# Kernel optimization log

Measured on AMD Instinct MI355X. Metric: run time of the kernel, lower is better.

Reference implementation:

```python
import jax, jax.numpy as jnp
import numpy as np

_CLIP = 1e4

def _n2n(t):
    return jnp.nan_to_num(t, nan=0.0, posinf=_CLIP, neginf=-_CLIP)

def setup_inputs() -> dict:
    key = jax.random.key(0)
    ks = jax.random.split(key, 9)
    B, N, E, DH, DM = 4, 16384, 65536, 128, 64
    s = 0.05
    return {
        "x": jax.random.normal(ks[0], (B, N, 3), jnp.float32),
        "h": jax.random.normal(ks[1], (B, N, DH), jnp.float32),
        "edge_index": jax.random.randint(ks[2], (B, E, 2), 0, N, jnp.int64 if jax.config.jax_enable_x64 else jnp.int32),
        "pe_w1": jax.random.normal(ks[3], (2 * DH + 1, DM), jnp.float32) * s,
        "pe_b1": jnp.zeros((DM,), jnp.float32),
        "pe_w2": jax.random.normal(ks[4], (DM, DM), jnp.float32) * s,
        "pe_b2": jnp.zeros((DM,), jnp.float32),
        "px_w": jax.random.normal(ks[5], (DM, 1), jnp.float32) * s,
        "ph_w1": jax.random.normal(ks[6], (DH + DM, DH), jnp.float32) * s,
        "ph_b1": jnp.zeros((DH,), jnp.float32),
        "ph_w2": jax.random.normal(ks[7], (DH, DH), jnp.float32) * s,
        "ph_b2": jnp.zeros((DH,), jnp.float32),
    }

def reference(x, h, edge_index, pe_w1, pe_b1, pe_w2, pe_b2, px_w, ph_w1, ph_b1, ph_w2, ph_b2):
    B = x.shape[0]
    src = edge_index[:, :, 0]          # [B,E]
    dst = edge_index[:, :, 1]
    bidx = jnp.arange(B)[:, None]      # [B,1] for batched gather/scatter
    x_i = x[bidx, src]                 # [B,E,3]
    x_j = x[bidx, dst]
    h_i = h[bidx, src]                 # [B,E,DH]
    h_j = h[bidx, dst]
    diff = x_i - x_j
    dist2 = jnp.clip((diff ** 2).sum(-1, keepdims=True), 1e-12, None)  # [B,E,1]
    edge_input = _n2n(jnp.concatenate([h_i, h_j, dist2], axis=-1))
    # phi_e: Linear -> SiLU -> Linear -> SiLU
    m = jax.nn.silu(edge_input @ pe_w1 + pe_b1)
    m_ij = _n2n(jax.nn.silu(m @ pe_w2 + pe_b2))   # [B,E,DM]
    m_x = m_ij @ px_w                             # [B,E,1]
    direction = diff / (jnp.sqrt(dist2) + 1e-8)
    delta_x_ij = _n2n(m_x * direction)            # [B,E,3]
    delta_x = jnp.zeros_like(x).at[bidx, src].add(delta_x_ij)
    delta_h_msg = jnp.zeros((B, x.shape[1], m_ij.shape[-1]), h.dtype).at[bidx, src].add(m_ij)
    h_input = jnp.concatenate([h, delta_h_msg], axis=-1)
    h_new = h + jax.nn.silu(h_input @ ph_w1 + ph_b1) @ ph_w2 + ph_b2
    x_new = x + delta_x
    return _n2n(x_new), _n2n(h_new)
```

## Files before the change

### kernel.cpp

```cpp
#include <hip/hip_runtime.h>


typedef unsigned short ushort_t;
typedef __attribute__((ext_vector_type(8))) short bf16x8;
typedef __attribute__((ext_vector_type(4))) float f32x4;
typedef _Float16 h2 __attribute__((ext_vector_type(2)));

__device__ __forceinline__ float fast_rcp(float v) { return __builtin_amdgcn_rcpf(v); }
__device__ __forceinline__ float fast_silu(float v) { return v * fast_rcp(1.0f + __expf(-v)); }
__device__ __forceinline__ ushort_t f2bf(float f) {
    unsigned u = __float_as_uint(f);
    u += 0x7fffu + ((u >> 16) & 1u);
    return (ushort_t)(u >> 16);
}
__device__ __forceinline__ float bf2f(ushort_t b) {
    return __uint_as_float(((unsigned)b) << 16);
}
__device__ __forceinline__ h2 u2h2(unsigned u) {
    union { unsigned u; h2 h; } v; v.u = u; return v.h;
}

__global__ __launch_bounds__(256) void init_k(const float* __restrict__ pe_w1,
                                              const float* __restrict__ pe_w2,
                                              const float* __restrict__ ph_w1,
                                              const float* __restrict__ ph_w2,
                                              int* __restrict__ cursor,
                                              ushort_t* __restrict__ W1t,
                                              ushort_t* __restrict__ Wp1t,
                                              ushort_t* __restrict__ Wp2t,
                                              unsigned* __restrict__ w2h) {
    int gg = blockIdx.x * 256 + threadIdx.x;
    if (gg < 65536) { cursor[gg] = 0; return; }
    int g = gg - 65536;
    if (g < 16384) {
        int c = g >> 7, k = g & 127;
        float v = (c < 64) ? pe_w1[k * 64 + c] : pe_w1[(128 + k) * 64 + (c - 64)];
        W1t[g] = f2bf(v);
    } else if (g < 40960) {
        int g2 = g - 16384;
        int n = g2 / 192, k = g2 - n * 192;
        Wp1t[g2] = f2bf(ph_w1[k * 128 + n]);
    } else if (g < 57344) {
        int g3 = g - 40960;
        int n = g3 >> 7, k = g3 & 127;
        Wp2t[g3] = f2bf(ph_w2[k * 128 + n]);
    } else if (g < 59392) {
        int g4 = g - 57344;
        int k2 = g4 >> 6, c = g4 & 63;
        union { unsigned u; _Float16 h[2]; } p;
        p.h[0] = (_Float16)pe_w2[(2 * k2) * 64 + c];
        p.h[1] = (_Float16)pe_w2[(2 * k2 + 1) * 64 + c];
        w2h[g4] = p.u;
    }
}

__global__ __launch_bounds__(256) void scatter_k(const int* __restrict__ ei,
                                                 int* __restrict__ cursor,
                                                 int* __restrict__ elist) {
    int e = blockIdx.x * 256 + threadIdx.x;
    int2 sd = ((const int2*)ei)[e];
    int b = e >> 16;
    int gi = (b << 14) + sd.x;
    int gj = (b << 14) + sd.y;
    int slot = atomicAdd(&cursor[gi], 1);
    if (slot < 64) elist[gi * 64 + slot] = gj;
}

__global__ __launch_bounds__(64, 4) void node_k(const float* __restrict__ x,
                                                const ushort_t* __restrict__ P,
                                                const int* __restrict__ cursor,
                                                const int* __restrict__ elist,
                                                const float* __restrict__ w1,
                                                const float* __restrict__ b1,
                                                const unsigned* __restrict__ w2h,
                                                const float* __restrict__ b2,
                                                const float* __restrict__ pxw,
                                                ushort_t* __restrict__ dh,
                                                float* __restrict__ outx) {
    const int n = blockIdx.x;
    const int lane = threadIdx.x;
    __shared__ __attribute__((aligned(16))) unsigned m_u[32];
    ushort_t* mh = (ushort_t*)m_u;

    const float w1r = w1[256 * 64 + lane];
    const float b2v = b2[lane];
    const float pxv = pxw[lane];
    const float Pib = bf2f(P[(size_t)n * 128 + lane]) + b1[lane];
    const float xi0 = x[n * 3 + 0];
    const float xi1 = x[n * 3 + 1];
    const float xi2 = x[n * 3 + 2];

    float dhacc = 0.0f;
    float dxp0 = 0.0f, dxp1 = 0.0f, dxp2 = 0.0f;
    const int dg = min(cursor[n], 64);
    const int base = n * 64;

    int gj0 = (dg > 0) ? elist[base] : 0;
    float Pj = bf2f(P[(size_t)gj0 * 128 + 64 + lane]);
    float xj0 = x[gj0 * 3 + 0];
    float xj1 = x[gj0 * 3 + 1];
    float xj2 = x[gj0 * 3 + 2];

    for (int t = 0; t < dg; t++) {
        int gjn = (t + 1 < dg) ? elist[base + t + 1] : 0;
        float Pjn = bf2f(P[(size_t)gjn * 128 + 64 + lane]);
        float xn0 = x[gjn * 3 + 0];
        float xn1 = x[gjn * 3 + 1];
        float xn2 = x[gjn * 3 + 2];

        float ddx = xi0 - xj0;
        float ddy = xi1 - xj1;
        float ddz = xi2 - xj2;
        float d2 = fmaxf(ddx * ddx + ddy * ddy + ddz * ddz, 1e-12f);
        float m = fast_silu(Pib + Pj + d2 * w1r);
        __builtin_amdgcn_wave_barrier();
        union { ushort_t s; _Float16 h; } mc;
        mc.h = (_Float16)m;
        mh[lane] = mc.s;
        __builtin_amdgcn_wave_barrier();
        float s0 = b2v, s1 = 0.0f, s2 = 0.0f, s3 = 0.0f;
#pragma unroll
        for (int q = 0; q < 8; q++) {
            uint4 mm = *(const uint4*)&m_u[q * 4];
            s0 = __builtin_amdgcn_fdot2(u2h2(mm.x), u2h2(w2h[(4 * q + 0) * 64 + lane]), s0, false);
            s1 = __builtin_amdgcn_fdot2(u2h2(mm.y), u2h2(w2h[(4 * q + 1) * 64 + lane]), s1, false);
            s2 = __builtin_amdgcn_fdot2(u2h2(mm.z), u2h2(w2h[(4 * q + 2) * 64 + lane]), s2, false);
            s3 = __builtin_amdgcn_fdot2(u2h2(mm.w), u2h2(w2h[(4 * q + 3) * 64 + lane]), s3, false);
        }
        __builtin_amdgcn_wave_barrier();
        float m2 = fast_silu((s0 + s1) + (s2 + s3));
        dhacc += m2;
        float c = m2 * pxv * fast_rcp(sqrtf(d2) + 1e-8f);
        dxp0 = fmaf(c, ddx, dxp0);
        dxp1 = fmaf(c, ddy, dxp1);
        dxp2 = fmaf(c, ddz, dxp2);

        Pj = Pjn; xj0 = xn0; xj1 = xn1; xj2 = xn2;
    }

    dh[(size_t)n * 64 + lane] = f2bf(dhacc);

    for (int off = 32; off; off >>= 1) {
        dxp0 += __shfl_down(dxp0, off);
        dxp1 += __shfl_down(dxp1, off);
        dxp2 += __shfl_down(dxp2, off);
    }
    if (lane == 0) {
        outx[n * 3 + 0] = xi0 + dxp0;
        outx[n * 3 + 1] = xi1 + dxp1;
        outx[n * 3 + 2] = xi2 + dxp2;
    }
}

template <bool EMIT_BF16>
__global__ __launch_bounds__(256, 2) void pgemm_k(const float* __restrict__ A0,
                                                  const ushort_t* __restrict__ Wt,
                                                  ushort_t* __restrict__ outP,
                                                  ushort_t* __restrict__ hbout) {
    constexpr int KPAD = 40;
    __shared__ ushort_t As[128 * KPAD];
    __shared__ ushort_t Bs[128 * KPAD];
    const int tid = threadIdx.x;
    const int m0 = blockIdx.x * 128;
    const int wave = tid >> 6;
    const int lane = tid & 63;
    const int lr = lane & 15;
    const int lq = lane >> 4;

    f32x4 acc[2][8];
#pragma unroll
    for (int mt = 0; mt < 2; mt++)
#pragma unroll
        for (int nt = 0; nt < 8; nt++) { f32x4 z = {0.f,0.f,0.f,0.f}; acc[mt][nt] = z; }

    for (int k0 = 0; k0 < 128; k0 += 32) {
#pragma unroll
        for (int i = 0; i < 4; i++) {
            int lin = tid + i * 256;
            int m = lin >> 3;
            int kq = (lin & 7) * 4;
            float4 v = *(const float4*)(A0 + (size_t)(m0 + m) * 128 + k0 + kq);
            ushort4 w4;
            w4.x = f2bf(v.x); w4.y = f2bf(v.y); w4.z = f2bf(v.z); w4.w = f2bf(v.w);
            if (EMIT_BF16)
                *(ushort4*)(hbout + (size_t)(m0 + m) * 128 + k0 + kq) = w4;
            *(ushort4*)&As[m * KPAD + kq] = w4;
        }
#pragma unroll
        for (int i = 0; i < 2; i++) {
            int lin = tid + i * 256;
            int n = lin >> 2;
            int kq = (lin & 3) * 8;
            *(uint4*)&Bs[n * KPAD + kq] = *(const uint4*)(Wt + (size_t)n * 128 + k0 + kq);
        }
        __syncthreads();
        bf16x8 af[2], bfr[8];
#pragma unroll
        for (int mt = 0; mt < 2; mt++)
            af[mt] = *(const bf16x8*)&As[(wave * 32 + mt * 16 + lr) * KPAD + lq * 8];
#pragma unroll
        for (int nt = 0; nt < 8; nt++)
            bfr[nt] = *(const bf16x8*)&Bs[(nt * 16 + lr) * KPAD + lq * 8];
#pragma unroll
        for (int mt = 0; mt < 2; mt++)
#pragma unroll
            for (int nt = 0; nt < 8; nt++)
                acc[mt][nt] = __builtin_amdgcn_mfma_f32_16x16x32_bf16(af[mt], bfr[nt], acc[mt][nt], 0, 0, 0);
        __syncthreads();
    }
#pragma unroll
    for (int mt = 0; mt < 2; mt++)
#pragma unroll
        for (int nt = 0; nt < 8; nt++)
#pragma unroll
            for (int r = 0; r < 4; r++) {
                int row = m0 + wave * 32 + mt * 16 + lq * 4 + r;
                int col = nt * 16 + lr;
                outP[(size_t)row * 128 + col] = f2bf(acc[mt][nt][r]);
            }
}

template <bool USE_HB>
__global__ __launch_bounds__(256, 2) void mlp_fused_k(const float* __restrict__ h,
                                                      const ushort_t* __restrict__ hb,
                                                      const ushort_t* __restrict__ dh,
                                                      const ushort_t* __restrict__ Wp1t,
                                                      const float* __restrict__ b1,
                                                      const ushort_t* __restrict__ Wp2t,
                                                      const float* __restrict__ b2,
                                                      float* __restrict__ outh) {
    constexpr int KPAD = 40, TPAD = 136;
    __shared__ ushort_t As[128 * KPAD];
    __shared__ ushort_t Bs[128 * KPAD];
    __shared__ ushort_t Ts[128 * TPAD];
    const int tid = threadIdx.x;
    const int m0 = blockIdx.x * 128;
    const int wave = tid >> 6;
    const int lane = tid & 63;
    const int lr = lane & 15;
    const int lq = lane >> 4;

    f32x4 acc[2][8];
#pragma unroll
    for (int mt = 0; mt < 2; mt++)
#pragma unroll
        for (int nt = 0; nt < 8; nt++) { f32x4 z = {0.f,0.f,0.f,0.f}; acc[mt][nt] = z; }

    for (int k0 = 0; k0 < 192; k0 += 32) {
        if (USE_HB) {
#pragma unroll
            for (int i = 0; i < 2; i++) {
                int lin = tid + i * 256;
                int m = lin >> 2;
                int kq = (lin & 3) * 8;
                const ushort_t* src = (k0 >= 128)
                    ? dh + (size_t)(m0 + m) * 64 + (k0 - 128 + kq)
                    : hb + (size_t)(m0 + m) * 128 + k0 + kq;
                *(uint4*)&As[m * KPAD + kq] = *(const uint4*)src;
            }
        } else {
#pragma unroll
            for (int i = 0; i < 4; i++) {
                int lin = tid + i * 256;
                int m = lin >> 3;
                int kq = (lin & 7) * 4;
                ushort4 w4;
                if (k0 >= 128) {
                    w4 = *(const ushort4*)(dh + (size_t)(m0 + m) * 64 + (k0 - 128 + kq));
                } else {
                    float4 v = *(const float4*)(h + (size_t)(m0 + m) * 128 + k0 + kq);
                    w4.x = f2bf(v.x); w4.y = f2bf(v.y); w4.z = f2bf(v.z); w4.w = f2bf(v.w);
                }
                *(ushort4*)&As[m * KPAD + kq] = w4;
            }
        }
#pragma unroll
        for (int i = 0; i < 2; i++) {
            int lin = tid + i * 256;
            int n = lin >> 2;
            int kq = (lin & 3) * 8;
            *(uint4*)&Bs[n * KPAD + kq] = *(const uint4*)(Wp1t + (size_t)n * 192 + k0 + kq);
        }
        __syncthreads();
        bf16x8 af[2], bfr[8];
#pragma unroll
        for (int mt = 0; mt < 2; mt++)
            af[mt] = *(const bf16x8*)&As[(wave * 32 + mt * 16 + lr) * KPAD + lq * 8];
#pragma unroll
        for (int nt = 0; nt < 8; nt++)
            bfr[nt] = *(const bf16x8*)&Bs[(nt * 16 + lr) * KPAD + lq * 8];
#pragma unroll
        for (int mt = 0; mt < 2; mt++)
#pragma unroll
            for (int nt = 0; nt < 8; nt++)
                acc[mt][nt] = __builtin_amdgcn_mfma_f32_16x16x32_bf16(af[mt], bfr[nt], acc[mt][nt], 0, 0, 0);
        __syncthreads();
    }
#pragma unroll
    for (int mt = 0; mt < 2; mt++)
#pragma unroll
        for (int nt = 0; nt < 8; nt++)
#pragma unroll
            for (int r = 0; r < 4; r++) {
                int row = wave * 32 + mt * 16 + lq * 4 + r;
                int col = nt * 16 + lr;
                Ts[row * TPAD + col] = f2bf(fast_silu(acc[mt][nt][r] + b1[col]));
            }
    __syncthreads();

    f32x4 acc2[2][8];
#pragma unroll
    for (int mt = 0; mt < 2; mt++)
#pragma unroll
        for (int nt = 0; nt < 8; nt++) { f32x4 z = {0.f,0.f,0.f,0.f}; acc2[mt][nt] = z; }

    for (int k0 = 0; k0 < 128; k0 += 32) {
#pragma unroll
        for (int i = 0; i < 2; i++) {
            int lin = tid + i * 256;
            int n = lin >> 2;
            int kq = (lin & 3) * 8;
            *(uint4*)&Bs[n * KPAD + kq] = *(const uint4*)(Wp2t + (size_t)n * 128 + k0 + kq);
        }
        __syncthreads();
        bf16x8 af[2], bfr[8];
#pragma unroll
        for (int mt = 0; mt < 2; mt++)
            af[mt] = *(const bf16x8*)&Ts[(wave * 32 + mt * 16 + lr) * TPAD + k0 + lq * 8];
#pragma unroll
        for (int nt = 0; nt < 8; nt++)
            bfr[nt] = *(const bf16x8*)&Bs[(nt * 16 + lr) * KPAD + lq * 8];
#pragma unroll
        for (int mt = 0; mt < 2; mt++)
#pragma unroll
            for (int nt = 0; nt < 8; nt++)
                acc2[mt][nt] = __builtin_amdgcn_mfma_f32_16x16x32_bf16(af[mt], bfr[nt], acc2[mt][nt], 0, 0, 0);
        __syncthreads();
    }
#pragma unroll
    for (int mt = 0; mt < 2; mt++)
#pragma unroll
        for (int nt = 0; nt < 8; nt++)
#pragma unroll
            for (int r = 0; r < 4; r++) {
                int row = m0 + wave * 32 + mt * 16 + lq * 4 + r;
                int col = nt * 16 + lr;
                float v = acc2[mt][nt][r] + b2[col];
                if (USE_HB) v += bf2f(hb[(size_t)row * 128 + col]);
                else        v += h[(size_t)row * 128 + col];
                outh[(size_t)row * 128 + col] = v;
            }
}

extern "C" void kernel_launch(void* const* d_in, const int* in_sizes, int n_in,
                              void* d_out, int out_size, void* d_ws, size_t ws_size,
                              hipStream_t stream) {
    const float* x     = (const float*)d_in[0];
    const float* h     = (const float*)d_in[1];
    const int*   ei    = (const int*)d_in[2];
    const float* pe_w1 = (const float*)d_in[3];
    const float* pe_b1 = (const float*)d_in[4];
    const float* pe_w2 = (const float*)d_in[5];
    const float* pe_b2 = (const float*)d_in[6];
    const float* px_w  = (const float*)d_in[7];
    const float* ph_w1 = (const float*)d_in[8];
    const float* ph_b1 = (const float*)d_in[9];
    const float* ph_w2 = (const float*)d_in[10];
    const float* ph_b2 = (const float*)d_in[11];

    float* outx = (float*)d_out;
    float* outh = (float*)d_out + 196608;

    ushort_t* P    = (ushort_t*)d_ws;
    ushort_t* dh   = P + (size_t)65536 * 128;
    int* cursor    = (int*)(dh + (size_t)65536 * 64);
    int* elist     = cursor + 65536;
    ushort_t* W1t  = (ushort_t*)(elist + (size_t)65536 * 64);
    ushort_t* Wp1t = W1t + 16384;
    ushort_t* Wp2t = Wp1t + 24576;
    unsigned* w2h  = (unsigned*)(Wp2t + 16384);
    ushort_t* hb   = (ushort_t*)(w2h + 4096);
    size_t need_hb = (size_t)((char*)(hb + (size_t)65536 * 128) - (char*)d_ws);
    const bool use_hb = ws_size >= need_hb;

    init_k<<<488, 256, 0, stream>>>(pe_w1, pe_w2, ph_w1, ph_w2,
                                    cursor, W1t, Wp1t, Wp2t, w2h);
    if (use_hb)
        pgemm_k<true><<<512, 256, 0, stream>>>(h, W1t, P, hb);
    else
        pgemm_k<false><<<512, 256, 0, stream>>>(h, W1t, P, nullptr);
    scatter_k<<<1024, 256, 0, stream>>>(ei, cursor, elist);
    node_k<<<65536, 64, 0, stream>>>(x, P, cursor, elist,
                                     pe_w1, pe_b1, w2h, pe_b2, px_w,
                                     dh, outx);
    if (use_hb)
        mlp_fused_k<true><<<512, 256, 0, stream>>>(h, hb, dh, Wp1t, ph_b1,
                                                   Wp2t, ph_b2, outh);
    else
        mlp_fused_k<false><<<512, 256, 0, stream>>>(h, nullptr, dh, Wp1t, ph_b1,
                                                    Wp2t, ph_b2, outh);
}
```

Measured before the change: 193.9 us.

## Fuse edge scatter into projection GEMM launch and drop LDS staging in node MLP

Merges the edge-bucketing scatter kernel into the projection GEMM launch as extra blocks, removing one kernel launch and letting the atomics overlap with the GEMM. Adds mlp_fast_k, which reads bf16 A and weight fragments straight from global memory into MFMA operands, with no LDS staging and no per-step barriers, and raises the occupancy hint to 3 blocks. The trade is uncoalesced, repeated global weight reads, which now lean on the cache, in exchange for less LDS traffic and no synchronisation. The residual still adds the bf16 copy of h, as the old path did.

```diff
diff --git a/kernel.cpp b/kernel.cpp
--- a/kernel.cpp
+++ b/kernel.cpp
@@ -54,16 +54,87 @@
     }
 }
 
-__global__ __launch_bounds__(256) void scatter_k(const int* __restrict__ ei,
-                                                 int* __restrict__ cursor,
-                                                 int* __restrict__ elist) {
-    int e = blockIdx.x * 256 + threadIdx.x;
-    int2 sd = ((const int2*)ei)[e];
-    int b = e >> 16;
-    int gi = (b << 14) + sd.x;
-    int gj = (b << 14) + sd.y;
-    int slot = atomicAdd(&cursor[gi], 1);
-    if (slot < 64) elist[gi * 64 + slot] = gj;
+template <bool EMIT_BF16>
+__global__ __launch_bounds__(256, 2) void pgemm_scatter_k(const float* __restrict__ A0,
+                                                          const ushort_t* __restrict__ Wt,
+                                                          ushort_t* __restrict__ outP,
+                                                          ushort_t* __restrict__ hbout,
+                                                          const int* __restrict__ ei,
+                                                          int* __restrict__ cursor,
+                                                          int* __restrict__ elist) {
+    constexpr int KPAD = 40;
+    __shared__ ushort_t As[128 * KPAD];
+    __shared__ ushort_t Bs[128 * KPAD];
+    const int tid = threadIdx.x;
+
+    if (blockIdx.x >= 512) {
+        int e = (blockIdx.x - 512) * 256 + tid;
+        int2 sd = ((const int2*)ei)[e];
+        int b = e >> 16;
+        int gi = (b << 14) + sd.x;
+        int gj = (b << 14) + sd.y;
+        int slot = atomicAdd(&cursor[gi], 1);
+        if (slot < 64) elist[gi * 64 + slot] = gj;
+        return;
+    }
+
+    const int m0 = blockIdx.x * 128;
+    const int wave = tid >> 6;
+    const int lane = tid & 63;
+    const int lr = lane & 15;
+    const int lq = lane >> 4;
+
+    f32x4 acc[2][8];
+#pragma unroll
+    for (int mt = 0; mt < 2; mt++)
+#pragma unroll
+        for (int nt = 0; nt < 8; nt++) { f32x4 z = {0.f,0.f,0.f,0.f}; acc[mt][nt] = z; }
+
+    for (int k0 = 0; k0 < 128; k0 += 32) {
+#pragma unroll
+        for (int i = 0; i < 4; i++) {
+            int lin = tid + i * 256;
+            int m = lin >> 3;
+            int kq = (lin & 7) * 4;
+            float4 v = *(const float4*)(A0 + (size_t)(m0 + m) * 128 + k0 + kq);
+            ushort4 w4;
+            w4.x = f2bf(v.x); w4.y = f2bf(v.y); w4.z = f2bf(v.z); w4.w = f2bf(v.w);
+            if (EMIT_BF16)
+                *(ushort4*)(hbout + (size_t)(m0 + m) * 128 + k0 + kq) = w4;
+            *(ushort4*)&As[m * KPAD + kq] = w4;
+        }
+#pragma unroll
+        for (int i = 0; i < 2; i++) {
+            int lin = tid + i * 256;
+            int n = lin >> 2;
+            int kq = (lin & 3) * 8;
+            *(uint4*)&Bs[n * KPAD + kq] = *(const uint4*)(Wt + (size_t)n * 128 + k0 + kq);
+        }
+        __syncthreads();
+        bf16x8 af[2], bfr[8];
+#pragma unroll
+        for (int mt = 0; mt < 2; mt++)
+            af[mt] = *(const bf16x8*)&As[(wave * 32 + mt * 16 + lr) * KPAD + lq * 8];
+#pragma unroll
+        for (int nt = 0; nt < 8; nt++)
+            bfr[nt] = *(const bf16x8*)&Bs[(nt * 16 + lr) * KPAD + lq * 8];
+#pragma unroll
+        for (int mt = 0; mt < 2; mt++)
+#pragma unroll
+            for (int nt = 0; nt < 8; nt++)
+                acc[mt][nt] = __builtin_amdgcn_mfma_f32_16x16x32_bf16(af[mt], bfr[nt], acc[mt][nt], 0, 0, 0);
+        __syncthreads();
+    }
+#pragma unroll
+    for (int mt = 0; mt < 2; mt++)
+#pragma unroll
+        for (int nt = 0; nt < 8; nt++)
+#pragma unroll
+            for (int r = 0; r < 4; r++) {
+                int row = m0 + wave * 32 + mt * 16 + lq * 4 + r;
+                int col = nt * 16 + lr;
+                outP[(size_t)row * 128 + col] = f2bf(acc[mt][nt][r]);
+            }
 }
 
 __global__ __launch_bounds__(64, 4) void node_k(const float* __restrict__ x,
@@ -152,14 +223,15 @@
     }
 }
 
-template <bool EMIT_BF16>
-__global__ __launch_bounds__(256, 2) void pgemm_k(const float* __restrict__ A0,
-                                                  const ushort_t* __restrict__ Wt,
-                                                  ushort_t* __restrict__ outP,
-                                                  ushort_t* __restrict__ hbout) {
-    constexpr int KPAD = 40;
-    __shared__ ushort_t As[128 * KPAD];
-    __shared__ ushort_t Bs[128 * KPAD];
+__global__ __launch_bounds__(256, 3) void mlp_fast_k(const ushort_t* __restrict__ hb,
+                                                     const ushort_t* __restrict__ dh,
+                                                     const ushort_t* __restrict__ Wp1t,
+                                                     const float* __restrict__ b1,
+                                                     const ushort_t* __restrict__ Wp2t,
+                                                     const float* __restrict__ b2,
+                                                     float* __restrict__ outh) {
+    constexpr int TPAD = 136;
+    __shared__ ushort_t Ts[128 * TPAD];
     const int tid = threadIdx.x;
     const int m0 = blockIdx.x * 128;
     const int wave = tid >> 6;
@@ -173,40 +245,54 @@
 #pragma unroll
         for (int nt = 0; nt < 8; nt++) { f32x4 z = {0.f,0.f,0.f,0.f}; acc[mt][nt] = z; }
 
-    for (int k0 = 0; k0 < 128; k0 += 32) {
-#pragma unroll
-        for (int i = 0; i < 4; i++) {
-            int lin = tid + i * 256;
-            int m = lin >> 3;
-            int kq = (lin & 7) * 4;
-            float4 v = *(const float4*)(A0 + (size_t)(m0 + m) * 128 + k0 + kq);
-            ushort4 w4;
-            w4.x = f2bf(v.x); w4.y = f2bf(v.y); w4.z = f2bf(v.z); w4.w = f2bf(v.w);
-            if (EMIT_BF16)
-                *(ushort4*)(hbout + (size_t)(m0 + m) * 128 + k0 + kq) = w4;
-            *(ushort4*)&As[m * KPAD + kq] = w4;
-        }
-#pragma unroll
-        for (int i = 0; i < 2; i++) {
-            int lin = tid + i * 256;
-            int n = lin >> 2;
-            int kq = (lin & 3) * 8;
-            *(uint4*)&Bs[n * KPAD + kq] = *(const uint4*)(Wt + (size_t)n * 128 + k0 + kq);
-        }
-        __syncthreads();
+    for (int k0 = 0; k0 < 192; k0 += 32) {
         bf16x8 af[2], bfr[8];
 #pragma unroll
-        for (int mt = 0; mt < 2; mt++)
-            af[mt] = *(const bf16x8*)&As[(wave * 32 + mt * 16 + lr) * KPAD + lq * 8];
-#pragma unroll
-        for (int nt = 0; nt < 8; nt++)
-            bfr[nt] = *(const bf16x8*)&Bs[(nt * 16 + lr) * KPAD + lq * 8];
+        for (int mt = 0; mt < 2; mt++) {
+            int row = m0 + wave * 32 + mt * 16 + lr;
+            af[mt] = (k0 < 128)
+                ? *(const bf16x8*)&hb[(size_t)row * 128 + k0 + lq * 8]
+                : *(const bf16x8*)&dh[(size_t)row * 64 + (k0 - 128) + lq * 8];
+        }
+#pragma unroll
+        for (int nt = 0; nt < 8; nt++)
+            bfr[nt] = *(const bf16x8*)&Wp1t[(size_t)(nt * 16 + lr) * 192 + k0 + lq * 8];
 #pragma unroll
         for (int mt = 0; mt < 2; mt++)
 #pragma unroll
             for (int nt = 0; nt < 8; nt++)
                 acc[mt][nt] = __builtin_amdgcn_mfma_f32_16x16x32_bf16(af[mt], bfr[nt], acc[mt][nt], 0, 0, 0);
-        __syncthreads();
+    }
+#pragma unroll
+    for (int mt = 0; mt < 2; mt++)
+#pragma unroll
+        for (int nt = 0; nt < 8; nt++)
+#pragma unroll
+            for (int r = 0; r < 4; r++) {
+                int row = wave * 32 + mt * 16 + lq * 4 + r;
+                int col = nt * 16 + lr;
+                Ts[row * TPAD + col] = f2bf(fast_silu(acc[mt][nt][r] + b1[col]));
+            }
+
+    f32x4 acc2[2][8];
+#pragma unroll
+    for (int mt = 0; mt < 2; mt++)
+#pragma unroll
+        for (int nt = 0; nt < 8; nt++) { f32x4 z = {0.f,0.f,0.f,0.f}; acc2[mt][nt] = z; }
+
+    for (int k0 = 0; k0 < 128; k0 += 32) {
+        bf16x8 af[2], bfr[8];
+#pragma unroll
+        for (int mt = 0; mt < 2; mt++)
+            af[mt] = *(const bf16x8*)&Ts[(wave * 32 + mt * 16 + lr) * TPAD + k0 + lq * 8];
+#pragma unroll
+        for (int nt = 0; nt < 8; nt++)
+            bfr[nt] = *(const bf16x8*)&Wp2t[(size_t)(nt * 16 + lr) * 128 + k0 + lq * 8];
+#pragma unroll
+        for (int mt = 0; mt < 2; mt++)
+#pragma unroll
+            for (int nt = 0; nt < 8; nt++)
+                acc2[mt][nt] = __builtin_amdgcn_mfma_f32_16x16x32_bf16(af[mt], bfr[nt], acc2[mt][nt], 0, 0, 0);
     }
 #pragma unroll
     for (int mt = 0; mt < 2; mt++)
@@ -216,13 +302,12 @@
             for (int r = 0; r < 4; r++) {
                 int row = m0 + wave * 32 + mt * 16 + lq * 4 + r;
                 int col = nt * 16 + lr;
-                outP[(size_t)row * 128 + col] = f2bf(acc[mt][nt][r]);
-            }
-}
-
-template <bool USE_HB>
+                float v = acc2[mt][nt][r] + b2[col] + bf2f(hb[(size_t)row * 128 + col]);
+                outh[(size_t)row * 128 + col] = v;
+            }
+}
+
 __global__ __launch_bounds__(256, 2) void mlp_fused_k(const float* __restrict__ h,
-                                                      const ushort_t* __restrict__ hb,
                                                       const ushort_t* __restrict__ dh,
                                                       const ushort_t* __restrict__ Wp1t,
                                                       const float* __restrict__ b1,
@@ -247,32 +332,19 @@
         for (int nt = 0; nt < 8; nt++) { f32x4 z = {0.f,0.f,0.f,0.f}; acc[mt][nt] = z; }
 
     for (int k0 = 0; k0 < 192; k0 += 32) {
-        if (USE_HB) {
-#pragma unroll
-            for (int i = 0; i < 2; i++) {
-                int lin = tid + i * 256;
-                int m = lin >> 2;
-                int kq = (lin & 3) * 8;
-                const ushort_t* src = (k0 >= 128)
-                    ? dh + (size_t)(m0 + m) * 64 + (k0 - 128 + kq)
-                    : hb + (size_t)(m0 + m) * 128 + k0 + kq;
-                *(uint4*)&As[m * KPAD + kq] = *(const uint4*)src;
-            }
-        } else {
-#pragma unroll
-            for (int i = 0; i < 4; i++) {
-                int lin = tid + i * 256;
-                int m = lin >> 3;
-                int kq = (lin & 7) * 4;
-                ushort4 w4;
-                if (k0 >= 128) {
-                    w4 = *(const ushort4*)(dh + (size_t)(m0 + m) * 64 + (k0 - 128 + kq));
-                } else {
-                    float4 v = *(const float4*)(h + (size_t)(m0 + m) * 128 + k0 + kq);
-                    w4.x = f2bf(v.x); w4.y = f2bf(v.y); w4.z = f2bf(v.z); w4.w = f2bf(v.w);
-                }
-                *(ushort4*)&As[m * KPAD + kq] = w4;
-            }
+#pragma unroll
+        for (int i = 0; i < 4; i++) {
+            int lin = tid + i * 256;
+            int m = lin >> 3;
+            int kq = (lin & 7) * 4;
+            ushort4 w4;
+            if (k0 >= 128) {
+                w4 = *(const ushort4*)(dh + (size_t)(m0 + m) * 64 + (k0 - 128 + kq));
+            } else {
+                float4 v = *(const float4*)(h + (size_t)(m0 + m) * 128 + k0 + kq);
+                w4.x = f2bf(v.x); w4.y = f2bf(v.y); w4.z = f2bf(v.z); w4.w = f2bf(v.w);
+            }
+            *(ushort4*)&As[m * KPAD + kq] = w4;
         }
 #pragma unroll
         for (int i = 0; i < 2; i++) {
@@ -345,9 +417,7 @@
             for (int r = 0; r < 4; r++) {
                 int row = m0 + wave * 32 + mt * 16 + lq * 4 + r;
                 int col = nt * 16 + lr;
-                float v = acc2[mt][nt][r] + b2[col];
-                if (USE_HB) v += bf2f(hb[(size_t)row * 128 + col]);
-                else        v += h[(size_t)row * 128 + col];
+                float v = acc2[mt][nt][r] + b2[col] + h[(size_t)row * 128 + col];
                 outh[(size_t)row * 128 + col] = v;
             }
 }
@@ -386,17 +456,18 @@
     init_k<<<488, 256, 0, stream>>>(pe_w1, pe_w2, ph_w1, ph_w2,
                                     cursor, W1t, Wp1t, Wp2t, w2h);
     if (use_hb)
-        pgemm_k<true><<<512, 256, 0, stream>>>(h, W1t, P, hb);
+        pgemm_scatter_k<true><<<1536, 256, 0, stream>>>(h, W1t, P, hb,
+                                                        ei, cursor, elist);
     else
-        pgemm_k<false><<<512, 256, 0, stream>>>(h, W1t, P, nullptr);
-    scatter_k<<<1024, 256, 0, stream>>>(ei, cursor, elist);
+        pgemm_scatter_k<false><<<1536, 256, 0, stream>>>(h, W1t, P, nullptr,
+                                                         ei, cursor, elist);
     node_k<<<65536, 64, 0, stream>>>(x, P, cursor, elist,
                                      pe_w1, pe_b1, w2h, pe_b2, px_w,
                                      dh, outx);
     if (use_hb)
-        mlp_fused_k<true><<<512, 256, 0, stream>>>(h, hb, dh, Wp1t, ph_b1,
-                                                   Wp2t, ph_b2, outh);
+        mlp_fast_k<<<512, 256, 0, stream>>>(hb, dh, Wp1t, ph_b1,
+                                            Wp2t, ph_b2, outh);
     else
-        mlp_fused_k<false><<<512, 256, 0, stream>>>(h, nullptr, dh, Wp1t, ph_b1,
-                                                    Wp2t, ph_b2, outh);
-}
+        mlp_fused_k<<<512, 256, 0, stream>>>(h, dh, Wp1t, ph_b1,
+                                             Wp2t, ph_b2, outh);
+}
```

New measurement: 201.7 us. 1.04x slower.
